# Kernel tuning notes

Measured on AMD Instinct MI355X. Metric: run time of the kernel, lower is better.

## Reference

```python
import jax, jax.numpy as jnp
import numpy as np
from jax import lax

# Problem dims (match init_kwargs / input_specs)
B, C, H, W = 4, 256, 64, 64
G, KH, KW, PAD = 8, 3, 3, 1
KK = KH * KW
CG = C // G  # channels per group


def setup_inputs() -> dict:
    key = jax.random.key(0)
    k0, k1, k2, k3, k4 = jax.random.split(key, 5)
    x = jax.random.normal(k0, (B, C, H, W), jnp.float32)
    # offset predictor conv: Conv2d(C, 2*KK*G, 3, padding=1); small init keeps offsets moderate
    offset_w = jax.random.normal(k1, (2 * KK * G, C, 3, 3), jnp.float32) * 0.01
    offset_b = jax.random.normal(k2, (2 * KK * G,), jnp.float32) * 0.01
    # deformable grouped conv weight: [C_out=C, C_in//G, KH, KW]
    fan_in = CG * KK
    deform_w = jax.random.normal(k3, (C, CG, KH, KW), jnp.float32) / np.sqrt(fan_in).astype(np.float32)
    deform_b = jax.random.normal(k4, (C,), jnp.float32) * 0.01
    return {"x": x, "offset_w": offset_w, "offset_b": offset_b,
            "deform_w": deform_w, "deform_b": deform_b}


def _deform_group_conv(x, offset_w, offset_b, deform_w, deform_b):
    # 1) predict offsets with a plain 3x3 conv
    offset = lax.conv_general_dilated(
        x, offset_w, window_strides=(1, 1), padding=((PAD, PAD), (PAD, PAD)),
        dimension_numbers=("NCHW", "OIHW", "NCHW")) + offset_b[None, :, None, None]

    # torchvision layout: [B, G, KK, (dy,dx), H, W]
    off = offset.reshape(B, G, KK, 2, H, W)
    off_y, off_x = off[:, :, :, 0], off[:, :, :, 1]  # [B,G,KK,H,W]

    dt = x.dtype
    hh = jnp.arange(H, dtype=dt)[None, None, None, :, None]
    ww = jnp.arange(W, dtype=dt)[None, None, None, None, :]
    ki = (jnp.arange(KK) // KW).astype(dt)[None, None, :, None, None]
    kj = (jnp.arange(KK) % KW).astype(dt)[None, None, :, None, None]
    # sampling coords for each (kernel tap, output location): [B,G,KK,H,W]
    py = hh - PAD + ki + off_y
    px = ww - PAD + kj + off_x

    y0f, x0f = jnp.floor(py), jnp.floor(px)
    wy1, wx1 = py - y0f, px - x0f
    wy0, wx0 = 1.0 - wy1, 1.0 - wx1
    iy0, ix0 = y0f.astype(jnp.int32), x0f.astype(jnp.int32)

    x_g = x.reshape(B, G, CG, H * W)
    # gather over flattened spatial dim, vmapped over (B, G)
    gather = jax.vmap(jax.vmap(lambda xf, idx: jnp.take(xf, idx, axis=1)))

    def corner(iy, ix, wgt):
        valid = (iy >= 0) & (iy < H) & (ix >= 0) & (ix < W)  # zero padding outside
        idx = (jnp.clip(iy, 0, H - 1) * W + jnp.clip(ix, 0, W - 1)).reshape(B, G, -1)
        w = (wgt * valid.astype(wgt.dtype)).reshape(B, G, 1, -1)
        return gather(x_g, idx) * w  # [B,G,CG,KK*H*W]

    sampled = (corner(iy0,     ix0,     wy0 * wx0)
             + corner(iy0,     ix0 + 1, wy0 * wx1)
             + corner(iy0 + 1, ix0,     wy1 * wx0)
             + corner(iy0 + 1, ix0 + 1, wy1 * wx1))
    sampled = sampled.reshape(B, G, CG, KK, H, W)

    # grouped conv as an einsum over (in-channels-per-group, kernel taps)
    w_g = deform_w.reshape(G, C // G, CG, KK)  # [G, out/g, in/g, KK]
    out = jnp.einsum("gock,bgckhw->bgohw", w_g, sampled).reshape(B, C, H, W)
    return out + deform_b[None, :, None, None]


def reference(x, offset_w, offset_b, deform_w, deform_b):
    return _deform_group_conv(x, offset_w, offset_b, deform_w, deform_b)
```

## Files before the change

### kernel.cpp

```cpp
#include <hip/hip_runtime.h>
#include <hip/hip_bf16.h>
#include <cstddef>
#include <cstdint>

#define CH_HW 4096

typedef __bf16  bf16x8  __attribute__((ext_vector_type(8)));
typedef float   f32x4   __attribute__((ext_vector_type(4)));
typedef unsigned int u32x4 __attribute__((ext_vector_type(4)));

#define WF_ELEMS 331776
#define WF_BYTES (WF_ELEMS * 2)
#define OFFW_BYTES (4u * 144u * CH_HW * 2u)
#define DWB_ELEMS (8 * 9 * 2 * 512)
#define DWB_BYTES (DWB_ELEMS * 2)
#define XT_BYTES ((size_t)4 * 8 * CH_HW * 32 * 2)

__device__ __forceinline__ u32x4 pack_bf16x8(const float av[8]) {
    u32x4 ad;
#pragma unroll
    for (int jj = 0; jj < 4; ++jj) {
        const unsigned int lo = __builtin_bit_cast(unsigned short, __float2bfloat16(av[2 * jj]));
        const unsigned int hi = __builtin_bit_cast(unsigned short, __float2bfloat16(av[2 * jj + 1]));
        ad[jj] = lo | (hi << 16);
    }
    return ad;
}
__device__ __forceinline__ float bf16lo(unsigned int u) {
    return __builtin_bit_cast(float, u << 16);
}
__device__ __forceinline__ float bf16hi(unsigned int u) {
    return __builtin_bit_cast(float, u & 0xFFFF0000u);
}

__global__ __launch_bounds__(256) void prep(const float* __restrict__ ow,
                                            const float* __restrict__ dw,
                                            const float* __restrict__ x,
                                            __hip_bfloat16* __restrict__ wf,
                                            __hip_bfloat16* __restrict__ dwb,
                                            __hip_bfloat16* __restrict__ xt)
{
    const int job = blockIdx.y;
    if (job == 0) {
        const int t = blockIdx.x * 256 + threadIdx.x;
        if (t >= WF_ELEMS) return;
        const int j    = t & 7;
        const int lane = (t >> 3) & 63;
        const int tmp  = t >> 9;
        const int nt   = tmp % 9;
        const int ks   = tmp / 9;
        const int tap  = ks >> 3, icb = ks & 7;
        const int oc   = nt * 16 + (lane & 15);
        const int ic   = icb * 32 + (lane >> 4) * 8 + j;
        wf[t] = __float2bfloat16(ow[(size_t)oc * 2304 + ic * 9 + tap]);
    } else if (job == 1) {
        const int t = blockIdx.x * 256 + threadIdx.x;
        if (t >= DWB_ELEMS) return;
        const int j    = t & 7;
        const int lane = (t >> 3) & 63;
        const int nt   = (t >> 9) & 1;
        const int gk   = t >> 10;
        const int k    = gk % 9;
        const int g    = gk / 9;
        const int oc   = g * 32 + nt * 16 + (lane & 15);
        const int c    = (lane >> 4) * 8 + j;
        dwb[t] = __float2bfloat16(dw[(size_t)oc * 288 + c * 9 + k]);
    } else {
        const int bid = blockIdx.x;
        if (bid >= 512) return;
        const int chunk = bid & 15;
        const int g = (bid >> 4) & 7, b = bid >> 7;
        const int pix = (chunk << 8) + threadIdx.x;
        const float* xs = x + ((size_t)b * 256 + g * 32) * CH_HW + pix;
        __hip_bfloat16* xp = xt + ((size_t)b * 8 + g) * 4 * CH_HW * 8;
#pragma unroll
        for (int q = 0; q < 4; ++q) {
            float av[8];
#pragma unroll
            for (int j = 0; j < 8; ++j) av[j] = xs[(size_t)(q * 8 + j) * CH_HW];
            *(u32x4*)(xp + ((size_t)q * CH_HW + pix) * 8) = pack_bf16x8(av);
        }
    }
}

template<int NT>
__device__ __forceinline__ void offs_body5(
    const __hip_bfloat16* __restrict__ xb,
    const __hip_bfloat16* __restrict__ wfl,
    const float* __restrict__ ob,
    __hip_bfloat16* __restrict__ offw_b,
    float* __restrict__ redbase,
    int hrow, int colbase, int lane, int ntBase, int kh)
{
    const int arow = lane & 15, cgrp = lane >> 4;
    const int ks0 = kh * 36;

    auto loadA1 = [&](int ks, int mt) -> u32x4 {
        const int tap = ks >> 3, icb = ks & 7;
        const int dy = tap / 3 - 1, dx = tap % 3 - 1;
        const int sh = hrow + dy, sw = colbase + mt * 16 + arow + dx;
        const bool valid = (sh >= 0) & (sh < 64) & (sw >= 0) & (sw < 64);
        const int spix = (min(max(sh, 0), 63) << 6) + min(max(sw, 0), 63);
        u32x4 a = *(const u32x4*)(xb + ((size_t)(icb * 4 + cgrp) * CH_HW + spix) * 8);
        if (!valid) a = (u32x4){0, 0, 0, 0};
        return a;
    };

    f32x4 acc[2][NT];
#pragma unroll
    for (int mt = 0; mt < 2; ++mt)
#pragma unroll
        for (int nt = 0; nt < NT; ++nt) acc[mt][nt] = (f32x4){0.f, 0.f, 0.f, 0.f};

    u32x4 a0[2], a1[2], b0[NT], b1[NT];
#pragma unroll
    for (int mt = 0; mt < 2; ++mt) {
        a0[mt] = loadA1(ks0 + 0, mt);
        a1[mt] = loadA1(ks0 + 1, mt);
    }
#pragma unroll
    for (int nt = 0; nt < NT; ++nt) {
        b0[nt] = *(const u32x4*)(wfl + (size_t)((ks0 + 0) * 9 + nt) * 512);
        b1[nt] = *(const u32x4*)(wfl + (size_t)((ks0 + 1) * 9 + nt) * 512);
    }

#pragma unroll 1
    for (int i = 0; i < 34; i += 2) {
        const int ks = ks0 + i;
#pragma unroll
        for (int mt = 0; mt < 2; ++mt) {
            const bf16x8 af = __builtin_bit_cast(bf16x8, a0[mt]);
#pragma unroll
            for (int nt = 0; nt < NT; ++nt)
                acc[mt][nt] = __builtin_amdgcn_mfma_f32_16x16x32_bf16(
                    af, __builtin_bit_cast(bf16x8, b0[nt]), acc[mt][nt], 0, 0, 0);
        }
#pragma unroll
        for (int mt = 0; mt < 2; ++mt) a0[mt] = loadA1(ks + 2, mt);
#pragma unroll
        for (int nt = 0; nt < NT; ++nt)
            b0[nt] = *(const u32x4*)(wfl + (size_t)((ks + 2) * 9 + nt) * 512);
#pragma unroll
        for (int mt = 0; mt < 2; ++mt) {
            const bf16x8 af = __builtin_bit_cast(bf16x8, a1[mt]);
#pragma unroll
            for (int nt = 0; nt < NT; ++nt)
                acc[mt][nt] = __builtin_amdgcn_mfma_f32_16x16x32_bf16(
                    af, __builtin_bit_cast(bf16x8, b1[nt]), acc[mt][nt], 0, 0, 0);
        }
#pragma unroll
        for (int mt = 0; mt < 2; ++mt) a1[mt] = loadA1(ks + 3, mt);
#pragma unroll
        for (int nt = 0; nt < NT; ++nt)
            b1[nt] = *(const u32x4*)(wfl + (size_t)((ks + 3) * 9 + nt) * 512);
    }
#pragma unroll
    for (int mt = 0; mt < 2; ++mt) {
        const bf16x8 af = __builtin_bit_cast(bf16x8, a0[mt]);
#pragma unroll
        for (int nt = 0; nt < NT; ++nt)
            acc[mt][nt] = __builtin_amdgcn_mfma_f32_16x16x32_bf16(
                af, __builtin_bit_cast(bf16x8, b0[nt]), acc[mt][nt], 0, 0, 0);
    }
#pragma unroll
    for (int mt = 0; mt < 2; ++mt) {
        const bf16x8 af = __builtin_bit_cast(bf16x8, a1[mt]);
#pragma unroll
        for (int nt = 0; nt < NT; ++nt)
            acc[mt][nt] = __builtin_amdgcn_mfma_f32_16x16x32_bf16(
                af, __builtin_bit_cast(bf16x8, b1[nt]), acc[mt][nt], 0, 0, 0);
    }

    if (kh == 1) {
#pragma unroll
        for (int mt = 0; mt < 2; ++mt)
#pragma unroll
            for (int nt = 0; nt < NT; ++nt)
                *(f32x4*)&redbase[((mt * NT + nt) * 64 + lane) * 4] = acc[mt][nt];
    }
    __syncthreads();
    if (kh == 0) {
#pragma unroll
        for (int mt = 0; mt < 2; ++mt) {
            const int pxb = hrow * 64 + colbase + mt * 16 + (cgrp << 2);
#pragma unroll
            for (int nt = 0; nt < NT; ++nt) {
                const f32x4 other = *(const f32x4*)&redbase[((mt * NT + nt) * 64 + lane) * 4];
                const int oc = (ntBase + nt) * 16 + arow;
                const float bias = ob[oc];
                float av[4];
#pragma unroll
                for (int r = 0; r < 4; ++r) av[r] = acc[mt][nt][r] + other[r] + bias;
                unsigned int p0 = (unsigned int)__builtin_bit_cast(unsigned short, __float2bfloat16(av[0])) |
                                  ((unsigned int)__builtin_bit_cast(unsigned short, __float2bfloat16(av[1])) << 16);
                unsigned int p1 = (unsigned int)__builtin_bit_cast(unsigned short, __float2bfloat16(av[2])) |
                                  ((unsigned int)__builtin_bit_cast(unsigned short, __float2bfloat16(av[3])) << 16);
                unsigned int* op = (unsigned int*)(offw_b + (size_t)oc * CH_HW + pxb);
                op[0] = p0; op[1] = p1;
            }
        }
    }
}

__global__ __launch_bounds__(256) void offs_mfma5(
    const __hip_bfloat16* __restrict__ xt,
    const __hip_bfloat16* __restrict__ wf,
    const float* __restrict__ ob,
    __hip_bfloat16* __restrict__ offw)
{
    __shared__ float red[4608];
    const int bid  = blockIdx.x;
    const int xcd  = bid & 7;
    const int b    = xcd >> 1;
    const int th   = xcd & 1;
    const int hrow = (bid >> 3) & 63;
    const int tid  = threadIdx.x;
    const int lane = tid & 63, wv = tid >> 6;
    const int nh   = wv & 1, kh = wv >> 1;
    const int ntBase = nh * 5;
    const int colbase = th * 32;

    const __hip_bfloat16* xb  = xt + (size_t)b * 8 * CH_HW * 32;
    const __hip_bfloat16* wfl = wf + (size_t)(ntBase * 64 + lane) * 8;
    __hip_bfloat16* offw_b = offw + (size_t)b * 144 * CH_HW;
    float* redbase = red + nh * 2560;

    if (nh == 0) offs_body5<5>(xb, wfl, ob, offw_b, redbase, hrow, colbase, lane, ntBase, kh);
    else         offs_body5<4>(xb, wfl, ob, offw_b, redbase, hrow, colbase, lane, ntBase, kh);
}

struct Samp { int iA, iB, iC, iD; float wA, wB, wC, wD; };

__device__ __forceinline__ Samp make_samp(float py, float px) {
    const float y0f = floorf(py), x0f = floorf(px);
    const int iy0 = (int)y0f, ix0 = (int)x0f;
    const int iy1 = iy0 + 1,  ix1 = ix0 + 1;
    const float fy1 = py - y0f, fx1 = px - x0f;
    const float fy0 = 1.f - fy1, fx0 = 1.f - fx1;
    const bool vy0 = (iy0 >= 0) & (iy0 < 64);
    const bool vy1 = (iy1 >= 0) & (iy1 < 64);
    const bool vx0 = (ix0 >= 0) & (ix0 < 64);
    const bool vx1 = (ix1 >= 0) & (ix1 < 64);
    const int cy0 = min(max(iy0, 0), 63), cy1 = min(max(iy1, 0), 63);
    const int cx0 = min(max(ix0, 0), 63), cx1 = min(max(ix1, 0), 63);
    Samp s;
    s.iA = (cy0 << 6) + cx0; s.iB = (cy0 << 6) + cx1;
    s.iC = (cy1 << 6) + cx0; s.iD = (cy1 << 6) + cx1;
    s.wA = (vy0 & vx0) ? fy0 * fx0 : 0.f;
    s.wB = (vy0 & vx1) ? fy0 * fx1 : 0.f;
    s.wC = (vy1 & vx0) ? fy1 * fx0 : 0.f;
    s.wD = (vy1 & vx1) ? fy1 * fx1 : 0.f;
    return s;
}

__global__ __launch_bounds__(256, 4) void deform6(
    const __hip_bfloat16* __restrict__ xt,
    const __hip_bfloat16* __restrict__ offw,
    const __hip_bfloat16* __restrict__ dwb,
    const float* __restrict__ db,
    float* __restrict__ out)
{
    const int bid  = blockIdx.x;
    const int pair = bid & 31;
    const int pt   = bid >> 5;
    const int b    = pair >> 3;
    const int g    = pair & 7;
    const int tid = threadIdx.x;
    const int lane = tid & 63, wave = tid >> 6;
    const int arow = lane & 15, cgrp = lane >> 4;
    const int px = (pt << 6) + (wave << 4) + arow;
    const int h = px >> 6, w = px & 63;

    const __hip_bfloat16* xg   = xt + (((size_t)b * 8 + g) * 4 + cgrp) * CH_HW * 8;
    const __hip_bfloat16* offp = offw + ((size_t)b * 144 + g * 18) * CH_HW + px;
    const __hip_bfloat16* wgb  = dwb + (size_t)g * 9 * 2 * 512 + lane * 8;

    f32x4 acc0 = (f32x4){0.f, 0.f, 0.f, 0.f};
    f32x4 acc1 = (f32x4){0.f, 0.f, 0.f, 0.f};

#pragma unroll
    for (int k = 0; k < 9; ++k) {
        const float oy = __bfloat162float(offp[(size_t)(2 * k) * CH_HW]);
        const float ox = __bfloat162float(offp[(size_t)(2 * k + 1) * CH_HW]);
        const Samp s = make_samp((float)(h - 1 + k / 3) + oy,
                                 (float)(w - 1 + k % 3) + ox);
        const u32x4 cA = *(const u32x4*)(xg + (size_t)s.iA * 8);
        const u32x4 cB = *(const u32x4*)(xg + (size_t)s.iB * 8);
        const u32x4 cC = *(const u32x4*)(xg + (size_t)s.iC * 8);
        const u32x4 cD = *(const u32x4*)(xg + (size_t)s.iD * 8);
        const u32x4 bu0 = *(const u32x4*)(wgb + (size_t)(k * 2 + 0) * 512);
        const u32x4 bu1 = *(const u32x4*)(wgb + (size_t)(k * 2 + 1) * 512);

        float v[8];
#pragma unroll
        for (int qq = 0; qq < 4; ++qq) {
            v[2 * qq] = s.wA * bf16lo(cA[qq]) + s.wB * bf16lo(cB[qq]) +
                        s.wC * bf16lo(cC[qq]) + s.wD * bf16lo(cD[qq]);
            v[2 * qq + 1] = s.wA * bf16hi(cA[qq]) + s.wB * bf16hi(cB[qq]) +
                            s.wC * bf16hi(cC[qq]) + s.wD * bf16hi(cD[qq]);
        }
        const bf16x8 afr = __builtin_bit_cast(bf16x8, pack_bf16x8(v));
        acc0 = __builtin_amdgcn_mfma_f32_16x16x32_bf16(
            afr, __builtin_bit_cast(bf16x8, bu0), acc0, 0, 0, 0);
        acc1 = __builtin_amdgcn_mfma_f32_16x16x32_bf16(
            afr, __builtin_bit_cast(bf16x8, bu1), acc1, 0, 0, 0);
    }

    const int pix4 = (pt << 6) + (wave << 4) + (cgrp << 2);
#pragma unroll
    for (int nt = 0; nt < 2; ++nt) {
        const f32x4 a = nt ? acc1 : acc0;
        const int oc = g * 32 + nt * 16 + arow;
        const float bias = db[oc];
        float4 o4;
        o4.x = a[0] + bias; o4.y = a[1] + bias;
        o4.z = a[2] + bias; o4.w = a[3] + bias;
        *(float4*)&out[((size_t)b * 256 + oc) * CH_HW + pix4] = o4;
    }
}

__device__ __forceinline__ void stageA_load(const float* __restrict__ xb,
                                            int hrow, int m, int kc, int ks,
                                            float av[8])
{
    const int tap = ks >> 3, icb = ks & 7;
    const int dy = tap / 3 - 1, dx = tap % 3 - 1;
    const int sh = hrow + dy, sw = m + dx;
    const float msk = (sh >= 0 && sh < 64 && sw >= 0 && sw < 64) ? 1.f : 0.f;
    const int shc = min(max(sh, 0), 63), swc = min(max(sw, 0), 63);
    const float* p = xb + (size_t)(icb * 32 + kc * 8) * CH_HW + (shc << 6) + swc;
#pragma unroll
    for (int j = 0; j < 8; ++j) av[j] = p[(size_t)j * CH_HW] * msk;
}

__global__ __launch_bounds__(256) void offs_mfma(const float* __restrict__ x,
                                                 const __hip_bfloat16* __restrict__ wf,
                                                 const float* __restrict__ ob,
                                                 __hip_bfloat16* __restrict__ offw)
{
    __shared__ __align__(16) unsigned short aL[2][64][40];
    __shared__ __align__(16) unsigned short bL[2][2560];

    const int bid  = blockIdx.x;
    const int nh   = bid & 1;
    const int hrow = (bid >> 1) & 63;
    const int b    = bid >> 7;
    const int ntBase = nh * 5;
    const int NTLOC  = 5 - nh;
    const int tid  = threadIdx.x;
    const int lane = tid & 63, wave = tid >> 6;
    const int m    = lane;
    const int kc   = wave;

    const float* xb = x + (size_t)b * 256 * CH_HW;

    f32x4 acc[5];
#pragma unroll
    for (int q = 0; q < 5; ++q) acc[q] = (f32x4){0.f, 0.f, 0.f, 0.f};

    {
        float av[8]; u32x4 bv[2];
        stageA_load(xb, hrow, m, kc, 0, av);
#pragma unroll
        for (int q = 0; q < 2; ++q) {
            const int ntl = wave + q * 4;
            if (ntl < NTLOC)
                bv[q] = *(const u32x4*)(wf + ((size_t)(ntBase + ntl) * 64 + lane) * 8);
        }
        *(u32x4*)&aL[0][m][kc * 8] = pack_bf16x8(av);
#pragma unroll
        for (int q = 0; q < 2; ++q) {
            const int ntl = wave + q * 4;
            if (ntl < NTLOC) *(u32x4*)&bL[0][ntl * 512 + lane * 8] = bv[q];
        }
    }
    __syncthreads();

    for (int ks = 0; ks < 72; ++ks) {
        const int buf = ks & 1, nbuf = buf ^ 1;
        const bool hasNext = (ks + 1) < 72;

        float av[8]; u32x4 bv[2];
        if (hasNext) {
            stageA_load(xb, hrow, m, kc, ks + 1, av);
#pragma unroll
            for (int q = 0; q < 2; ++q) {
                const int ntl = wave + q * 4;
                if (ntl < NTLOC)
                    bv[q] = *(const u32x4*)(wf + ((size_t)((ks + 1) * 9 + ntBase + ntl) * 64 + lane) * 8);
            }
        }

        const u32x4 au = *(const u32x4*)&aL[buf][wave * 16 + (lane & 15)][(lane >> 4) * 8];
        const bf16x8 afr = __builtin_bit_cast(bf16x8, au);
#pragma unroll
        for (int ntl = 0; ntl < 5; ++ntl) {
            if (ntl < NTLOC) {
                const u32x4 bu = *(const u32x4*)&bL[buf][ntl * 512 + lane * 8];
                acc[ntl] = __builtin_amdgcn_mfma_f32_16x16x32_bf16(
                    afr, __builtin_bit_cast(bf16x8, bu), acc[ntl], 0, 0, 0);
            }
        }

        if (hasNext) {
            *(u32x4*)&aL[nbuf][m][kc * 8] = pack_bf16x8(av);
#pragma unroll
            for (int q = 0; q < 2; ++q) {
                const int ntl = wave + q * 4;
                if (ntl < NTLOC) *(u32x4*)&bL[nbuf][ntl * 512 + lane * 8] = bv[q];
            }
        }
        __syncthreads();
    }

    const int oc_l = lane & 15;
    const int mrow = wave * 16 + ((lane >> 4) << 2);
#pragma unroll
    for (int ntl = 0; ntl < 5; ++ntl) {
        if (ntl < NTLOC) {
            const int oc = (ntBase + ntl) * 16 + oc_l;
            const float bias = ob[oc];
            __hip_bfloat16* op = offw + ((size_t)b * 144 + oc) * CH_HW + hrow * 64 + mrow;
#pragma unroll
            for (int r = 0; r < 4; ++r)
                op[r] = __float2bfloat16(acc[ntl][r] + bias);
        }
    }
}

__global__ __launch_bounds__(256) void deform3(const float* __restrict__ x,
                                               const __hip_bfloat16* __restrict__ offw,
                                               const __hip_bfloat16* __restrict__ dwb,
                                               const float* __restrict__ db,
                                               float* __restrict__ out)
{
    const int pt = blockIdx.x;
    const int g  = blockIdx.y;
    const int b  = blockIdx.z;
    const int tid  = threadIdx.x;
    const int lane = tid & 63, wave = tid >> 6;
    const int pixbase = (pt << 7) + (wave << 5);
    const int arow = lane & 15;
    const int cgrp = lane >> 4;

    const float* xg = x + ((size_t)b * 256 + g * 32 + cgrp * 8) * CH_HW;
    const __hip_bfloat16* offp = offw + ((size_t)b * 144 + g * 18) * CH_HW;
    const __hip_bfloat16* wgb = dwb + (size_t)g * 9 * 2 * 512;

    f32x4 acc[2][2];
#pragma unroll
    for (int mt = 0; mt < 2; ++mt)
#pragma unroll
        for (int nt = 0; nt < 2; ++nt) acc[mt][nt] = (f32x4){0.f, 0.f, 0.f, 0.f};

#pragma unroll 1
    for (int k = 0; k < 9; ++k) {
        const u32x4 bu0 = *(const u32x4*)(wgb + (size_t)(k * 2 + 0) * 512 + lane * 8);
        const u32x4 bu1 = *(const u32x4*)(wgb + (size_t)(k * 2 + 1) * 512 + lane * 8);
        const bf16x8 bf0 = __builtin_bit_cast(bf16x8, bu0);
        const bf16x8 bf1 = __builtin_bit_cast(bf16x8, bu1);
        const int ki = k / 3, kj = k % 3;

#pragma unroll
        for (int mt = 0; mt < 2; ++mt) {
            const int pix = pixbase + mt * 16 + arow;
            const int h = pix >> 6, w = pix & 63;
            const float oy = __bfloat162float(offp[(2 * k) * CH_HW + pix]);
            const float ox = __bfloat162float(offp[(2 * k + 1) * CH_HW + pix]);
            const Samp s = make_samp((float)(h - 1 + ki) + oy,
                                     (float)(w - 1 + kj) + ox);
            float v[8];
#pragma unroll
            for (int j = 0; j < 8; ++j) {
                const float* xc = xg + (size_t)j * CH_HW;
                v[j] = s.wA * xc[s.iA] + s.wB * xc[s.iB] +
                       s.wC * xc[s.iC] + s.wD * xc[s.iD];
            }
            const bf16x8 afr = __builtin_bit_cast(bf16x8, pack_bf16x8(v));
            acc[mt][0] = __builtin_amdgcn_mfma_f32_16x16x32_bf16(afr, bf0, acc[mt][0], 0, 0, 0);
            acc[mt][1] = __builtin_amdgcn_mfma_f32_16x16x32_bf16(afr, bf1, acc[mt][1], 0, 0, 0);
        }
    }

    const int ocl = lane & 15;
#pragma unroll
    for (int mt = 0; mt < 2; ++mt)
#pragma unroll
        for (int nt = 0; nt < 2; ++nt) {
            const int oc = g * 32 + nt * 16 + ocl;
            const float bias = db[oc];
            const int pix = pixbase + mt * 16 + ((lane >> 4) << 2);
            float4 o4;
            o4.x = acc[mt][nt][0] + bias;
            o4.y = acc[mt][nt][1] + bias;
            o4.z = acc[mt][nt][2] + bias;
            o4.w = acc[mt][nt][3] + bias;
            *(float4*)&out[((size_t)b * 256 + oc) * CH_HW + pix] = o4;
        }
}

extern "C" void kernel_launch(void* const* d_in, const int* in_sizes, int n_in,
                              void* d_out, int out_size, void* d_ws, size_t ws_size,
                              hipStream_t stream) {
    const float* x  = (const float*)d_in[0];
    const float* ow = (const float*)d_in[1];
    const float* ob = (const float*)d_in[2];
    const float* dw = (const float*)d_in[3];
    const float* db = (const float*)d_in[4];
    float* out = (float*)d_out;

    __hip_bfloat16* wf   = (__hip_bfloat16*)d_ws;
    __hip_bfloat16* offw = (__hip_bfloat16*)((char*)d_ws + WF_BYTES);
    __hip_bfloat16* dwb  = (__hip_bfloat16*)((char*)d_ws + WF_BYTES + OFFW_BYTES);
    __hip_bfloat16* xt   = (__hip_bfloat16*)((char*)d_ws + WF_BYTES + OFFW_BYTES + DWB_BYTES);

    const size_t needed = (size_t)WF_BYTES + OFFW_BYTES + DWB_BYTES + XT_BYTES;
    const int nblk = (WF_ELEMS + 255) / 256;

    if (ws_size >= needed) {
        prep<<<dim3(nblk, 3, 1), 256, 0, stream>>>(ow, dw, x, wf, dwb, xt);
        offs_mfma5<<<512, 256, 0, stream>>>(xt, wf, ob, offw);
        deform6<<<2048, 256, 0, stream>>>(xt, offw, dwb, db, out);
    } else {
        prep<<<dim3(nblk, 2, 1), 256, 0, stream>>>(ow, dw, x, wf, dwb, xt);
        offs_mfma<<<512, 256, 0, stream>>>(x, wf, ob, offw);
        deform3<<<dim3(32, 8, 4), 256, 0, stream>>>(x, offw, dwb, db, out);
    }
}
```

Measured before the change: 57.17 us.

## Split offset conv K dimension four ways and double block count

The offset-predictor MFMA kernel now splits its 72-step reduction across four waves of 18 steps each, where before it was split two ways across 36 steps. The N-tile halves move from waves to separate blocks, so the grid doubles to 1024 blocks. Three partial sums are reduced through a larger shared buffer, and launch bounds request 4 blocks per CU. The aim is more parallelism and shorter serial MFMA chains, at the cost of more shared-memory reduction traffic and more redundant A loads across blocks.

```diff
diff --git a/kernel.cpp b/kernel.cpp
--- a/kernel.cpp
+++ b/kernel.cpp
@@ -84,16 +84,16 @@
 }
 
 template<int NT>
-__device__ __forceinline__ void offs_body5(
+__device__ __forceinline__ void offs_body6(
     const __hip_bfloat16* __restrict__ xb,
     const __hip_bfloat16* __restrict__ wfl,
     const float* __restrict__ ob,
     __hip_bfloat16* __restrict__ offw_b,
-    float* __restrict__ redbase,
+    float* __restrict__ red,
     int hrow, int colbase, int lane, int ntBase, int kh)
 {
     const int arow = lane & 15, cgrp = lane >> 4;
-    const int ks0 = kh * 36;
+    const int ks0 = kh * 18;
 
     auto loadA1 = [&](int ks, int mt) -> u32x4 {
         const int tap = ks >> 3, icb = ks & 7;
@@ -125,7 +125,7 @@
     }
 
 #pragma unroll 1
-    for (int i = 0; i < 34; i += 2) {
+    for (int i = 0; i < 16; i += 2) {
         const int ks = ks0 + i;
 #pragma unroll
         for (int mt = 0; mt < 2; ++mt) {
@@ -171,12 +171,13 @@
                 af, __builtin_bit_cast(bf16x8, b1[nt]), acc[mt][nt], 0, 0, 0);
     }
 
-    if (kh == 1) {
+    if (kh > 0) {
+        float* r = red + (kh - 1) * 2560;
 #pragma unroll
         for (int mt = 0; mt < 2; ++mt)
 #pragma unroll
             for (int nt = 0; nt < NT; ++nt)
-                *(f32x4*)&redbase[((mt * NT + nt) * 64 + lane) * 4] = acc[mt][nt];
+                *(f32x4*)&r[((mt * NT + nt) * 64 + lane) * 4] = acc[mt][nt];
     }
     __syncthreads();
     if (kh == 0) {
@@ -185,48 +186,53 @@
             const int pxb = hrow * 64 + colbase + mt * 16 + (cgrp << 2);
 #pragma unroll
             for (int nt = 0; nt < NT; ++nt) {
-                const f32x4 other = *(const f32x4*)&redbase[((mt * NT + nt) * 64 + lane) * 4];
+                const int ri = ((mt * NT + nt) * 64 + lane) * 4;
+                const f32x4 p1 = *(const f32x4*)&red[ri];
+                const f32x4 p2 = *(const f32x4*)&red[2560 + ri];
+                const f32x4 p3 = *(const f32x4*)&red[5120 + ri];
                 const int oc = (ntBase + nt) * 16 + arow;
                 const float bias = ob[oc];
                 float av[4];
 #pragma unroll
-                for (int r = 0; r < 4; ++r) av[r] = acc[mt][nt][r] + other[r] + bias;
-                unsigned int p0 = (unsigned int)__builtin_bit_cast(unsigned short, __float2bfloat16(av[0])) |
+                for (int r4 = 0; r4 < 4; ++r4)
+                    av[r4] = acc[mt][nt][r4] + p1[r4] + p2[r4] + p3[r4] + bias;
+                unsigned int q0 = (unsigned int)__builtin_bit_cast(unsigned short, __float2bfloat16(av[0])) |
                                   ((unsigned int)__builtin_bit_cast(unsigned short, __float2bfloat16(av[1])) << 16);
-                unsigned int p1 = (unsigned int)__builtin_bit_cast(unsigned short, __float2bfloat16(av[2])) |
+                unsigned int q1 = (unsigned int)__builtin_bit_cast(unsigned short, __float2bfloat16(av[2])) |
                                   ((unsigned int)__builtin_bit_cast(unsigned short, __float2bfloat16(av[3])) << 16);
                 unsigned int* op = (unsigned int*)(offw_b + (size_t)oc * CH_HW + pxb);
-                op[0] = p0; op[1] = p1;
+                op[0] = q0; op[1] = q1;
             }
         }
     }
 }
 
-__global__ __launch_bounds__(256) void offs_mfma5(
+__global__ __launch_bounds__(256, 4) void offs_mfma6(
     const __hip_bfloat16* __restrict__ xt,
     const __hip_bfloat16* __restrict__ wf,
     const float* __restrict__ ob,
     __hip_bfloat16* __restrict__ offw)
 {
-    __shared__ float red[4608];
+    __shared__ float red[7680];
     const int bid  = blockIdx.x;
     const int xcd  = bid & 7;
     const int b    = xcd >> 1;
-    const int th   = xcd & 1;
-    const int hrow = (bid >> 3) & 63;
+    const int half = xcd & 1;
+    const int flat = half * 128 + (bid >> 3);
+    const int hrow = flat >> 2;
+    const int col  = (flat >> 1) & 1;
+    const int nh   = flat & 1;
     const int tid  = threadIdx.x;
-    const int lane = tid & 63, wv = tid >> 6;
-    const int nh   = wv & 1, kh = wv >> 1;
+    const int lane = tid & 63, kh = tid >> 6;
     const int ntBase = nh * 5;
-    const int colbase = th * 32;
+    const int colbase = col * 32;
 
     const __hip_bfloat16* xb  = xt + (size_t)b * 8 * CH_HW * 32;
     const __hip_bfloat16* wfl = wf + (size_t)(ntBase * 64 + lane) * 8;
     __hip_bfloat16* offw_b = offw + (size_t)b * 144 * CH_HW;
-    float* redbase = red + nh * 2560;
-
-    if (nh == 0) offs_body5<5>(xb, wfl, ob, offw_b, redbase, hrow, colbase, lane, ntBase, kh);
-    else         offs_body5<4>(xb, wfl, ob, offw_b, redbase, hrow, colbase, lane, ntBase, kh);
+
+    if (nh == 0) offs_body6<5>(xb, wfl, ob, offw_b, red, hrow, colbase, lane, ntBase, kh);
+    else         offs_body6<4>(xb, wfl, ob, offw_b, red, hrow, colbase, lane, ntBase, kh);
 }
 
 struct Samp { int iA, iB, iC, iD; float wA, wB, wC, wD; };
@@ -519,7 +525,7 @@
 
     if (ws_size >= needed) {
         prep<<<dim3(nblk, 3, 1), 256, 0, stream>>>(ow, dw, x, wf, dwb, xt);
-        offs_mfma5<<<512, 256, 0, stream>>>(xt, wf, ob, offw);
+        offs_mfma6<<<1024, 256, 0, stream>>>(xt, wf, ob, offw);
         deform6<<<2048, 256, 0, stream>>>(xt, offw, dwb, db, out);
     } else {
         prep<<<dim3(nblk, 2, 1), 256, 0, stream>>>(ow, dw, x, wf, dwb, xt);
```

Result: no change. 57.26 us (+0.2%).
